# Optimization experiments

Measured on AMD Instinct MI355X. Metric: run time of the kernel, lower is better.

The kernel has to match this reference:

```python
import jax, jax.numpy as jnp
import numpy as np

IN_DIMS = 1024
K = 8


def setup_inputs() -> dict:
    key = jax.random.key(0)
    ks = jax.random.split(key, 7)
    s = 1.0 / np.sqrt(IN_DIMS)
    x = jax.random.normal(ks[0], (8, 2048, IN_DIMS), dtype=jnp.float32)
    Wq = jax.random.uniform(ks[1], (IN_DIMS, K), jnp.float32, -s, s)
    bq = jax.random.uniform(ks[2], (K,), jnp.float32, -s, s)
    Wk = jax.random.uniform(ks[3], (IN_DIMS, K), jnp.float32, -s, s)
    bk = jax.random.uniform(ks[4], (K,), jnp.float32, -s, s)
    Wv = jax.random.uniform(ks[5], (IN_DIMS, IN_DIMS), jnp.float32, -s, s)
    bv = jax.random.uniform(ks[6], (IN_DIMS,), jnp.float32, -s, s)
    return {"x": x, "Wq": Wq, "bq": bq, "Wk": Wk, "bk": bk, "Wv": Wv, "bv": bv}


def reference(x, Wq, bq, Wk, bk, Wv, bv):
    # x: [B,S,D]; rank-k projections
    q = jnp.einsum('bsd,dk->bsk', x, Wq) + bq        # [B,S,k]
    k = jnp.einsum('bsd,dk->bsk', x, Wk) + bk        # [B,S,k]
    energy = jnp.einsum('bik,bjk->bij', q, k)        # [B,S,S] (unscaled)
    attention = jax.nn.softmax(energy, axis=-1)
    value = jnp.einsum('bsd,de->bse', x, Wv) + bv    # [B,S,D]
    out = jnp.einsum('bij,bjd->bid', attention, value)
    return (out, attention)
```

## Files before the change

kernel.cpp:

```cpp
#include <hip/hip_runtime.h>


typedef __attribute__((ext_vector_type(8))) __bf16 bf16x8;
typedef __attribute__((ext_vector_type(4))) __bf16 bf16x4;
typedef __attribute__((ext_vector_type(4))) float  f32x4;
typedef unsigned int u32;

#define GLB_CAST(p) ((const __attribute__((address_space(1))) u32*)(p))
#define LDS_CAST(p) ((__attribute__((address_space(3))) u32*)(p))

#define S_BARRIER() { __builtin_amdgcn_s_barrier(); __builtin_amdgcn_sched_barrier(0); }
#define VMCNT8()    { asm volatile("s_waitcnt vmcnt(8)" ::: "memory"); __builtin_amdgcn_sched_barrier(0); }
#define VMCNT0()    { asm volatile("s_waitcnt vmcnt(0)" ::: "memory"); __builtin_amdgcn_sched_barrier(0); }

static constexpr int    Bn   = 8;
static constexpr int    S    = 2048;
static constexpr int    Dd   = 1024;
static constexpr int    Mtot = Bn * S;
static constexpr size_t OUT0 = (size_t)Bn * S * Dd;

static constexpr size_t OFF_XBF  = 0;
static constexpr size_t OFF_WVT  = OFF_XBF  + (size_t)Mtot * Dd * 2;
static constexpr size_t OFF_WQKT = OFF_WVT  + (size_t)Dd * Dd * 2;
static constexpr size_t OFF_Q    = OFF_WQKT + (size_t)16 * Dd * 2;
static constexpr size_t OFF_K    = OFF_Q    + (size_t)Mtot * 8 * 4;
static constexpr size_t OFF_VT   = OFF_K    + (size_t)Mtot * 8 * 4;
static constexpr size_t OFF_ATTB = OFF_VT   + (size_t)Bn * Dd * S * 2;
static constexpr size_t WS_NEED  = OFF_ATTB + (size_t)Bn * S * S * 2;

__global__ __launch_bounds__(256) void prep_kernel(
    const float* __restrict__ x, const float* __restrict__ Wq,
    const float* __restrict__ Wk, const float* __restrict__ Wv,
    __bf16* __restrict__ xbf, __bf16* __restrict__ wvt, __bf16* __restrict__ wqkT)
{
    __shared__ float lt[64][65];
    int bid = blockIdx.x, t = threadIdx.x;
    if (bid < 4096) {
        #pragma unroll
        for (int i = 0; i < 4; ++i) {
            size_t idx4 = (size_t)i * 1048576 + (size_t)bid * 256 + t;
            f32x4 v = ((const f32x4*)x)[idx4];
            bf16x4 o;
            #pragma unroll
            for (int c = 0; c < 4; ++c) o[c] = (__bf16)v[c];
            ((bf16x4*)xbf)[idx4] = o;
        }
    } else if (bid < 4352) {
        int tile = bid - 4096;
        int tr = tile >> 4, tc = tile & 15;
        int r0 = t >> 6, c = t & 63;
        #pragma unroll
        for (int i = 0; i < 16; ++i) {
            int row = i * 4 + r0;
            lt[row][c] = Wv[(size_t)(tr * 64 + row) * 1024 + tc * 64 + c];
        }
        __syncthreads();
        #pragma unroll
        for (int i = 0; i < 16; ++i) {
            int er = i * 4 + r0;
            wvt[(size_t)(tc * 64 + er) * 1024 + tr * 64 + c] = (__bf16)lt[c][er];
        }
    } else {
        int lb = bid - 4352;
        #pragma unroll
        for (int i = 0; i < 4; ++i) {
            int idx = (lb * 4 + i) * 256 + t;
            int n = idx >> 10, d = idx & 1023;
            float v = (n < 8) ? Wq[d * 8 + n] : Wk[d * 8 + (n & 7)];
            wqkT[n * 1024 + d] = (__bf16)v;
        }
    }
}

__global__ __launch_bounds__(256) void qk_proj_kernel(
    const __bf16* __restrict__ xbf, const __bf16* __restrict__ wqkT,
    const float* __restrict__ bq, const float* __restrict__ bk,
    float* __restrict__ qb, float* __restrict__ kb)
{
    int t = threadIdx.x, l = t & 63, w = t >> 6;
    int mbase = (blockIdx.x * 4 + w) * 16;
    f32x4 acc = {0.f, 0.f, 0.f, 0.f};
    const __bf16* ar = xbf + (size_t)(mbase + (l & 15)) * 1024 + ((l >> 4) << 3);
    const __bf16* br = wqkT + (size_t)(l & 15) * 1024 + ((l >> 4) << 3);
    #pragma unroll 8
    for (int kk = 0; kk < 1024; kk += 32) {
        bf16x8 a = *(const bf16x8*)(ar + kk);
        bf16x8 b = *(const bf16x8*)(br + kk);
        acc = __builtin_amdgcn_mfma_f32_16x16x32_bf16(a, b, acc, 0, 0, 0);
    }
    int n = l & 15;
    float bias = (n < 8) ? bq[n] : bk[n & 7];
    #pragma unroll
    for (int r = 0; r < 4; ++r) {
        int m = mbase + ((l >> 4) << 2) + r;
        float v = acc[r] + bias;
        if (n < 8) qb[m * 8 + n] = v;
        else       kb[m * 8 + (n & 7)] = v;
    }
}

__global__ __launch_bounds__(256) void softmax_kernel(
    const float* __restrict__ qb, const float* __restrict__ kb,
    float* __restrict__ attnF, __bf16* __restrict__ attnB)
{
    int bid = blockIdx.x;
    int b = bid >> 6, chunk = bid & 63;
    int t = threadIdx.x, l = t & 63, w = t >> 6;
    float kr[8][8];
    const float* kbb = kb + ((size_t)b << 14);
    #pragma unroll
    for (int jj = 0; jj < 8; ++jj) {
        f32x4 v0 = *(const f32x4*)(kbb + (size_t)(t * 8 + jj) * 8);
        f32x4 v1 = *(const f32x4*)(kbb + (size_t)(t * 8 + jj) * 8 + 4);
        #pragma unroll
        for (int c = 0; c < 4; ++c) { kr[jj][c] = v0[c]; kr[jj][4 + c] = v1[c]; }
    }
    __shared__ float redm[4], reds[4];
    const float* qrow = qb + ((size_t)b << 14);
    for (int ii = 0; ii < 32; ++ii) {
        int i = (chunk << 5) + ii;
        f32x4 q0 = *(const f32x4*)(qrow + (size_t)i * 8);
        f32x4 q1 = *(const f32x4*)(qrow + (size_t)i * 8 + 4);
        float e[8];
        #pragma unroll
        for (int jj = 0; jj < 8; ++jj) {
            float s = q0[0] * kr[jj][0];
            s = fmaf(q0[1], kr[jj][1], s);
            s = fmaf(q0[2], kr[jj][2], s);
            s = fmaf(q0[3], kr[jj][3], s);
            s = fmaf(q1[0], kr[jj][4], s);
            s = fmaf(q1[1], kr[jj][5], s);
            s = fmaf(q1[2], kr[jj][6], s);
            s = fmaf(q1[3], kr[jj][7], s);
            e[jj] = s;
        }
        float mx = e[0];
        #pragma unroll
        for (int jj = 1; jj < 8; ++jj) mx = fmaxf(mx, e[jj]);
        #pragma unroll
        for (int d = 1; d < 64; d <<= 1) mx = fmaxf(mx, __shfl_xor(mx, d));
        if (l == 0) redm[w] = mx;
        __syncthreads();
        mx = fmaxf(fmaxf(redm[0], redm[1]), fmaxf(redm[2], redm[3]));
        float p[8], sum = 0.f;
        #pragma unroll
        for (int jj = 0; jj < 8; ++jj) { p[jj] = __expf(e[jj] - mx); sum += p[jj]; }
        #pragma unroll
        for (int d = 1; d < 64; d <<= 1) sum += __shfl_xor(sum, d);
        if (l == 0) reds[w] = sum;
        __syncthreads();
        float T = (reds[0] + reds[1]) + (reds[2] + reds[3]);
        float inv = 1.0f / T;
        size_t off = (((size_t)b << 11) + i) * 2048 + (size_t)t * 8;
        f32x4 o0, o1; bf16x8 ob;
        #pragma unroll
        for (int c = 0; c < 4; ++c) {
            o0[c] = p[c] * inv; o1[c] = p[4 + c] * inv;
            ob[c] = (__bf16)o0[c]; ob[4 + c] = (__bf16)o1[c];
        }
        *(f32x4*)(attnF + off) = o0;
        *(f32x4*)(attnF + off + 4) = o1;
        *(bf16x8*)(attnB + off) = ob;
    }
}

template<int LDA>
__device__ __forceinline__ void stage_tile(const __bf16* Ab, const __bf16* Bb,
    char* smem, int slot, int kk, int rowin, int sl8, int wid)
{
    #pragma unroll
    for (int r = 0; r < 4; ++r) {
        __builtin_amdgcn_global_load_lds(
            GLB_CAST(Ab + (size_t)(r * 64 + rowin) * LDA + kk + sl8 * 8),
            LDS_CAST(smem + slot * 65536 + r * 8192 + wid * 1024), 16, 0, 0);
        __builtin_amdgcn_global_load_lds(
            GLB_CAST(Bb + (size_t)(r * 64 + rowin) * LDA + kk + sl8 * 8),
            LDS_CAST(smem + slot * 65536 + 32768 + r * 8192 + wid * 1024), 16, 0, 0);
    }
}

template<int MODE>
__global__ __launch_bounds__(512, 2) void gemm_kernel(
    const __bf16* __restrict__ A, const __bf16* __restrict__ Bt,
    float* __restrict__ outF, __bf16* __restrict__ outVt,
    const float* __restrict__ bv)
{
    constexpr int LDA = (MODE == 0) ? 1024 : 2048;
    constexpr int NT  = LDA / 64;
    __shared__ __align__(1024) char smem[131072];

    int bid = blockIdx.x;
    int wg = ((bid & 7) << 5) | (bid >> 3);
    int t = threadIdx.x, l = t & 63;
    int wid = t >> 6;
    int wmr = wid >> 2, wnc = wid & 3;

    int mblk, nblk, bb = 0;
    size_t aoff, boff;
    if constexpr (MODE == 0) {
        mblk = wg >> 2; nblk = wg & 3;
        aoff = (size_t)mblk * 256 * LDA; boff = 0;
    } else {
        bb = wg >> 5; int r = wg & 31;
        mblk = r >> 2; nblk = r & 3;
        aoff = (size_t)bb * S * S + (size_t)mblk * 256 * LDA;
        boff = (size_t)bb * Dd * S;
    }
    const __bf16* Ab = A + aoff;
    const __bf16* Bb = Bt + boff + (size_t)nblk * 256 * LDA;

    int rowin = t >> 3;
    int sl8 = (t & 7) ^ (rowin & 7);
    int lr = l & 15, lk = l >> 4;

    f32x4 acc[8][4] = {};

    stage_tile<LDA>(Ab, Bb, smem, 0, 0, rowin, sl8, wid);
    stage_tile<LDA>(Ab, Bb, smem, 1, 64, rowin, sl8, wid);
    VMCNT8();
    S_BARRIER();

    for (int tt = 0; tt < NT; ++tt) {
        int s = tt & 1;
        const __bf16* Asl = (const __bf16*)(smem + s * 65536);
        const __bf16* Bsl = (const __bf16*)(smem + s * 65536 + 32768);
        #pragma unroll
        for (int ks = 0; ks < 2; ++ks) {
            int sa = ks * 4 + lk;
            bf16x8 af[8], bfr[4];
            #pragma unroll
            for (int i = 0; i < 8; ++i) {
                int ra = wmr * 128 + i * 16 + lr;
                af[i] = *(const bf16x8*)&Asl[ra * 64 + ((sa ^ (ra & 7)) << 3)];
            }
            #pragma unroll
            for (int j = 0; j < 4; ++j) {
                int rb = wnc * 64 + j * 16 + lr;
                bfr[j] = *(const bf16x8*)&Bsl[rb * 64 + ((sa ^ (rb & 7)) << 3)];
            }
            __builtin_amdgcn_s_setprio(1);
            #pragma unroll
            for (int i = 0; i < 8; ++i)
                #pragma unroll
                for (int j = 0; j < 4; ++j)
                    acc[i][j] = __builtin_amdgcn_mfma_f32_16x16x32_bf16(af[i], bfr[j], acc[i][j], 0, 0, 0);
            __builtin_amdgcn_s_setprio(0);
        }
        if (tt == NT - 1) break;
        S_BARRIER();
        if (tt + 2 < NT) {
            stage_tile<LDA>(Ab, Bb, smem, s, (tt + 2) * 64, rowin, sl8, wid);
            VMCNT8();
        } else {
            VMCNT0();
        }
        S_BARRIER();
    }

    if constexpr (MODE == 0) {
        #pragma unroll
        for (int j = 0; j < 4; ++j) {
            int e = (nblk << 8) + wnc * 64 + j * 16 + lr;
            float bias = bv[e];
            #pragma unroll
            for (int i = 0; i < 8; ++i) {
                int m0 = (mblk << 8) + wmr * 128 + i * 16 + (lk << 2);
                int b = m0 >> 11, s0 = m0 & 2047;
                bf16x4 o;
                #pragma unroll
                for (int r = 0; r < 4; ++r) o[r] = (__bf16)(acc[i][j][r] + bias);
                *(bf16x4*)&outVt[(((size_t)(b << 10) + e) << 11) + s0] = o;
            }
        }
    } else {
        float* ob = outF + (size_t)bb * S * Dd;
        #pragma unroll
        for (int i = 0; i < 8; ++i) {
            int m0 = (mblk << 8) + wmr * 128 + i * 16 + (lk << 2);
            #pragma unroll
            for (int j = 0; j < 4; ++j) {
                int e = (nblk << 8) + wnc * 64 + j * 16 + lr;
                #pragma unroll
                for (int r = 0; r < 4; ++r)
                    ob[(size_t)(m0 + r) * 1024 + e] = acc[i][j][r];
            }
        }
    }
}

extern "C" void kernel_launch(void* const* d_in, const int* in_sizes, int n_in,
                              void* d_out, int out_size, void* d_ws, size_t ws_size,
                              hipStream_t stream)
{
    const float* x  = (const float*)d_in[0];
    const float* Wq = (const float*)d_in[1];
    const float* bq = (const float*)d_in[2];
    const float* Wk = (const float*)d_in[3];
    const float* bk = (const float*)d_in[4];
    const float* Wv = (const float*)d_in[5];
    const float* bv = (const float*)d_in[6];

    float* outp  = (float*)d_out;
    float* attnF = outp + OUT0;

    if (ws_size < WS_NEED) return;
    char* ws = (char*)d_ws;
    __bf16* xbf   = (__bf16*)(ws + OFF_XBF);
    __bf16* wvt   = (__bf16*)(ws + OFF_WVT);
    __bf16* wqkT  = (__bf16*)(ws + OFF_WQKT);
    float*  qbuf  = (float*)(ws + OFF_Q);
    float*  kbuf  = (float*)(ws + OFF_K);
    __bf16* vt    = (__bf16*)(ws + OFF_VT);
    __bf16* attnB = (__bf16*)(ws + OFF_ATTB);

    prep_kernel<<<4368, 256, 0, stream>>>(x, Wq, Wk, Wv, xbf, wvt, wqkT);
    qk_proj_kernel<<<256, 256, 0, stream>>>(xbf, wqkT, bq, bk, qbuf, kbuf);
    gemm_kernel<0><<<256, 512, 0, stream>>>(xbf, wvt, nullptr, vt, bv);
    softmax_kernel<<<512, 256, 0, stream>>>(qbuf, kbuf, attnF, attnB);
    gemm_kernel<1><<<256, 512, 0, stream>>>(attnB, vt, outp, nullptr, nullptr);
}
```

Before: 198.0 us.

## Split GEMM main loop into four quadrant phases interleaving prefetch with MFMA

The GEMM inner loop now splits the 8x4 MFMA tile into four quadrants. Each quadrant's LDS fragment reads are issued before the previous quadrant's MFMAs. The next tile's global-to-LDS loads are scattered across the phases once each slot's data has been consumed, instead of issued as a block after all compute. The aim is to overlap LDS reads and global prefetch with matrix math, at the cost of many more barriers per iteration and a finer-grained schedule that relies on correct slot reuse ordering.

Result: no change. 196.3 us (-0.9%).

```diff
diff --git a/kernel.cpp b/kernel.cpp
--- a/kernel.cpp
+++ b/kernel.cpp
@@ -10,6 +10,7 @@
 #define LDS_CAST(p) ((__attribute__((address_space(3))) u32*)(p))
 
 #define S_BARRIER() { __builtin_amdgcn_s_barrier(); __builtin_amdgcn_sched_barrier(0); }
+#define LGKM0()     { asm volatile("s_waitcnt lgkmcnt(0)" ::: "memory"); __builtin_amdgcn_sched_barrier(0); }
 #define VMCNT8()    { asm volatile("s_waitcnt vmcnt(8)" ::: "memory"); __builtin_amdgcn_sched_barrier(0); }
 #define VMCNT0()    { asm volatile("s_waitcnt vmcnt(0)" ::: "memory"); __builtin_amdgcn_sched_barrier(0); }
 
@@ -165,18 +166,20 @@
 }
 
 template<int LDA>
-__device__ __forceinline__ void stage_tile(const __bf16* Ab, const __bf16* Bb,
-    char* smem, int slot, int kk, int rowin, int sl8, int wid)
-{
-    #pragma unroll
-    for (int r = 0; r < 4; ++r) {
-        __builtin_amdgcn_global_load_lds(
-            GLB_CAST(Ab + (size_t)(r * 64 + rowin) * LDA + kk + sl8 * 8),
-            LDS_CAST(smem + slot * 65536 + r * 8192 + wid * 1024), 16, 0, 0);
-        __builtin_amdgcn_global_load_lds(
-            GLB_CAST(Bb + (size_t)(r * 64 + rowin) * LDA + kk + sl8 * 8),
-            LDS_CAST(smem + slot * 65536 + 32768 + r * 8192 + wid * 1024), 16, 0, 0);
-    }
+__device__ __forceinline__ void stageA(const __bf16* Ab, char* smem,
+    int slot, int kk, int c, int rowin, int sl8, int wid)
+{
+    __builtin_amdgcn_global_load_lds(
+        GLB_CAST(Ab + (size_t)(c * 64 + rowin) * LDA + kk + sl8 * 8),
+        LDS_CAST(smem + slot * 65536 + c * 8192 + wid * 1024), 16, 0, 0);
+}
+template<int LDA>
+__device__ __forceinline__ void stageB(const __bf16* Bb, char* smem,
+    int slot, int kk, int c, int rowin, int sl8, int wid)
+{
+    __builtin_amdgcn_global_load_lds(
+        GLB_CAST(Bb + (size_t)(c * 64 + rowin) * LDA + kk + sl8 * 8),
+        LDS_CAST(smem + slot * 65536 + 32768 + c * 8192 + wid * 1024), 16, 0, 0);
 }
 
 template<int MODE>
@@ -215,8 +218,16 @@
 
     f32x4 acc[8][4] = {};
 
-    stage_tile<LDA>(Ab, Bb, smem, 0, 0, rowin, sl8, wid);
-    stage_tile<LDA>(Ab, Bb, smem, 1, 64, rowin, sl8, wid);
+    #pragma unroll
+    for (int c = 0; c < 4; ++c) {
+        stageA<LDA>(Ab, smem, 0, 0, c, rowin, sl8, wid);
+        stageB<LDA>(Bb, smem, 0, 0, c, rowin, sl8, wid);
+    }
+    #pragma unroll
+    for (int c = 0; c < 4; ++c) {
+        stageA<LDA>(Ab, smem, 1, 64, c, rowin, sl8, wid);
+        stageB<LDA>(Bb, smem, 1, 64, c, rowin, sl8, wid);
+    }
     VMCNT8();
     S_BARRIER();
 
@@ -224,36 +235,106 @@
         int s = tt & 1;
         const __bf16* Asl = (const __bf16*)(smem + s * 65536);
         const __bf16* Bsl = (const __bf16*)(smem + s * 65536 + 32768);
+        bool pf = (tt + 2 < NT);
+        int kk2 = (tt + 2) * 64;
+
+        bf16x8 aLo[2][4], aHi[2][4], bLo[2][2], bHi[2][2];
+
         #pragma unroll
         for (int ks = 0; ks < 2; ++ks) {
             int sa = ks * 4 + lk;
-            bf16x8 af[8], bfr[4];
-            #pragma unroll
-            for (int i = 0; i < 8; ++i) {
+            #pragma unroll
+            for (int i = 0; i < 4; ++i) {
                 int ra = wmr * 128 + i * 16 + lr;
-                af[i] = *(const bf16x8*)&Asl[ra * 64 + ((sa ^ (ra & 7)) << 3)];
-            }
-            #pragma unroll
-            for (int j = 0; j < 4; ++j) {
+                aLo[ks][i] = *(const bf16x8*)&Asl[ra * 64 + ((sa ^ (ra & 7)) << 3)];
+            }
+            #pragma unroll
+            for (int j = 0; j < 2; ++j) {
                 int rb = wnc * 64 + j * 16 + lr;
-                bfr[j] = *(const bf16x8*)&Bsl[rb * 64 + ((sa ^ (rb & 7)) << 3)];
-            }
-            __builtin_amdgcn_s_setprio(1);
-            #pragma unroll
-            for (int i = 0; i < 8; ++i)
-                #pragma unroll
-                for (int j = 0; j < 4; ++j)
-                    acc[i][j] = __builtin_amdgcn_mfma_f32_16x16x32_bf16(af[i], bfr[j], acc[i][j], 0, 0, 0);
-            __builtin_amdgcn_s_setprio(0);
-        }
+                bLo[ks][j] = *(const bf16x8*)&Bsl[rb * 64 + ((sa ^ (rb & 7)) << 3)];
+            }
+        }
+        S_BARRIER(); LGKM0();
+        __builtin_amdgcn_s_setprio(1);
+        #pragma unroll
+        for (int ks = 0; ks < 2; ++ks)
+            #pragma unroll
+            for (int i = 0; i < 4; ++i)
+                #pragma unroll
+                for (int j = 0; j < 2; ++j)
+                    acc[i][j] = __builtin_amdgcn_mfma_f32_16x16x32_bf16(aLo[ks][i], bLo[ks][j], acc[i][j], 0, 0, 0);
+        __builtin_amdgcn_s_setprio(0);
+        S_BARRIER();
+
+        #pragma unroll
+        for (int ks = 0; ks < 2; ++ks) {
+            int sa = ks * 4 + lk;
+            #pragma unroll
+            for (int j = 0; j < 2; ++j) {
+                int rb = wnc * 64 + (j + 2) * 16 + lr;
+                bHi[ks][j] = *(const bf16x8*)&Bsl[rb * 64 + ((sa ^ (rb & 7)) << 3)];
+            }
+        }
+        if (pf) {
+            stageA<LDA>(Ab, smem, s, kk2, 0, rowin, sl8, wid);
+            stageA<LDA>(Ab, smem, s, kk2, 2, rowin, sl8, wid);
+        }
+        S_BARRIER(); LGKM0();
+        __builtin_amdgcn_s_setprio(1);
+        #pragma unroll
+        for (int ks = 0; ks < 2; ++ks)
+            #pragma unroll
+            for (int i = 0; i < 4; ++i)
+                #pragma unroll
+                for (int j = 0; j < 2; ++j)
+                    acc[i][2 + j] = __builtin_amdgcn_mfma_f32_16x16x32_bf16(aLo[ks][i], bHi[ks][j], acc[i][2 + j], 0, 0, 0);
+        __builtin_amdgcn_s_setprio(0);
+        S_BARRIER();
+
+        #pragma unroll
+        for (int ks = 0; ks < 2; ++ks) {
+            int sa = ks * 4 + lk;
+            #pragma unroll
+            for (int i = 0; i < 4; ++i) {
+                int ra = wmr * 128 + (i + 4) * 16 + lr;
+                aHi[ks][i] = *(const bf16x8*)&Asl[ra * 64 + ((sa ^ (ra & 7)) << 3)];
+            }
+        }
+        if (pf) {
+            #pragma unroll
+            for (int c = 0; c < 4; ++c)
+                stageB<LDA>(Bb, smem, s, kk2, c, rowin, sl8, wid);
+        }
+        S_BARRIER(); LGKM0();
+        __builtin_amdgcn_s_setprio(1);
+        #pragma unroll
+        for (int ks = 0; ks < 2; ++ks)
+            #pragma unroll
+            for (int i = 0; i < 4; ++i)
+                #pragma unroll
+                for (int j = 0; j < 2; ++j)
+                    acc[4 + i][2 + j] = __builtin_amdgcn_mfma_f32_16x16x32_bf16(aHi[ks][i], bHi[ks][j], acc[4 + i][2 + j], 0, 0, 0);
+        __builtin_amdgcn_s_setprio(0);
+        S_BARRIER();
+
+        if (pf) {
+            stageA<LDA>(Ab, smem, s, kk2, 1, rowin, sl8, wid);
+            stageA<LDA>(Ab, smem, s, kk2, 3, rowin, sl8, wid);
+        }
+        S_BARRIER();
+        __builtin_amdgcn_s_setprio(1);
+        #pragma unroll
+        for (int ks = 0; ks < 2; ++ks)
+            #pragma unroll
+            for (int i = 0; i < 4; ++i)
+                #pragma unroll
+                for (int j = 0; j < 2; ++j)
+                    acc[4 + i][j] = __builtin_amdgcn_mfma_f32_16x16x32_bf16(aHi[ks][i], bLo[ks][j], acc[4 + i][j], 0, 0, 0);
+        __builtin_amdgcn_s_setprio(0);
+
         if (tt == NT - 1) break;
         S_BARRIER();
-        if (tt + 2 < NT) {
-            stage_tile<LDA>(Ab, Bb, smem, s, (tt + 2) * 64, rowin, sl8, wid);
-            VMCNT8();
-        } else {
-            VMCNT0();
-        }
+        if (pf) { VMCNT8(); } else { VMCNT0(); }
         S_BARRIER();
     }
 
```

## Fuse QK projection into prep kernel and precompute GEMM LDS/global addresses

Applied to the files above, without the earlier changes.

Removes the separate qk_proj kernel and the wqkT transpose: the Q/K projection now runs inside prep_kernel, reading fp32 x directly and gathering Wq/Wk columns with strided loads converted to bf16 on the fly. This saves one kernel launch and a dependency on xbf. In the GEMM kernel, swizzled LDS offsets and global row pointers are hoisted out of the main loop to cut per-iteration address arithmetic. The cost is strided, uncoalesced weight loads in the projection blocks and some extra register pressure from the hoisted pointers.

New measurement: 200.1 us. No clear change (+1.1%).

```diff
diff --git a/kernel.cpp b/kernel.cpp
--- a/kernel.cpp
+++ b/kernel.cpp
@@ -20,33 +20,51 @@
 static constexpr size_t OUT0 = (size_t)Bn * S * Dd;
 
 static constexpr size_t OFF_XBF  = 0;
-static constexpr size_t OFF_WVT  = OFF_XBF  + (size_t)Mtot * Dd * 2;
-static constexpr size_t OFF_WQKT = OFF_WVT  + (size_t)Dd * Dd * 2;
-static constexpr size_t OFF_Q    = OFF_WQKT + (size_t)16 * Dd * 2;
-static constexpr size_t OFF_K    = OFF_Q    + (size_t)Mtot * 8 * 4;
-static constexpr size_t OFF_VT   = OFF_K    + (size_t)Mtot * 8 * 4;
-static constexpr size_t OFF_ATTB = OFF_VT   + (size_t)Bn * Dd * S * 2;
+static constexpr size_t OFF_WVT  = OFF_XBF + (size_t)Mtot * Dd * 2;
+static constexpr size_t OFF_Q    = OFF_WVT + (size_t)Dd * Dd * 2;
+static constexpr size_t OFF_K    = OFF_Q   + (size_t)Mtot * 8 * 4;
+static constexpr size_t OFF_VT   = OFF_K   + (size_t)Mtot * 8 * 4;
+static constexpr size_t OFF_ATTB = OFF_VT  + (size_t)Bn * Dd * S * 2;
 static constexpr size_t WS_NEED  = OFF_ATTB + (size_t)Bn * S * S * 2;
 
 __global__ __launch_bounds__(256) void prep_kernel(
     const float* __restrict__ x, const float* __restrict__ Wq,
     const float* __restrict__ Wk, const float* __restrict__ Wv,
-    __bf16* __restrict__ xbf, __bf16* __restrict__ wvt, __bf16* __restrict__ wqkT)
+    const float* __restrict__ bq, const float* __restrict__ bk,
+    __bf16* __restrict__ xbf, __bf16* __restrict__ wvt,
+    float* __restrict__ qb, float* __restrict__ kb)
 {
     __shared__ float lt[64][65];
     int bid = blockIdx.x, t = threadIdx.x;
-    if (bid < 4096) {
-        #pragma unroll
-        for (int i = 0; i < 4; ++i) {
-            size_t idx4 = (size_t)i * 1048576 + (size_t)bid * 256 + t;
-            f32x4 v = ((const f32x4*)x)[idx4];
-            bf16x4 o;
-            #pragma unroll
-            for (int c = 0; c < 4; ++c) o[c] = (__bf16)v[c];
-            ((bf16x4*)xbf)[idx4] = o;
-        }
-    } else if (bid < 4352) {
-        int tile = bid - 4096;
+    if (bid < 256) {
+        int l = t & 63, w = t >> 6;
+        int mbase = (bid * 4 + w) * 16;
+        int n = l & 15;
+        int dbase = (l >> 4) << 3;
+        const float* xr = x + (size_t)(mbase + n) * 1024 + dbase;
+        const float* wcol = (n < 8) ? (Wq + n) : (Wk + (n & 7));
+        f32x4 acc = {0.f, 0.f, 0.f, 0.f};
+        #pragma unroll 4
+        for (int kk = 0; kk < 1024; kk += 32) {
+            f32x4 a0 = *(const f32x4*)(xr + kk);
+            f32x4 a1 = *(const f32x4*)(xr + kk + 4);
+            bf16x8 a, b;
+            #pragma unroll
+            for (int c = 0; c < 4; ++c) { a[c] = (__bf16)a0[c]; a[4 + c] = (__bf16)a1[c]; }
+            #pragma unroll
+            for (int u = 0; u < 8; ++u) b[u] = (__bf16)wcol[(size_t)(dbase + kk + u) * 8];
+            acc = __builtin_amdgcn_mfma_f32_16x16x32_bf16(a, b, acc, 0, 0, 0);
+        }
+        float bias = (n < 8) ? bq[n] : bk[n & 7];
+        #pragma unroll
+        for (int r = 0; r < 4; ++r) {
+            int m = mbase + ((l >> 4) << 2) + r;
+            float v = acc[r] + bias;
+            if (n < 8) qb[m * 8 + n] = v;
+            else       kb[m * 8 + (n & 7)] = v;
+        }
+    } else if (bid < 512) {
+        int tile = bid - 256;
         int tr = tile >> 4, tc = tile & 15;
         int r0 = t >> 6, c = t & 63;
         #pragma unroll
@@ -61,41 +79,16 @@
             wvt[(size_t)(tc * 64 + er) * 1024 + tr * 64 + c] = (__bf16)lt[c][er];
         }
     } else {
-        int lb = bid - 4352;
+        int bid2 = bid - 512;
         #pragma unroll
         for (int i = 0; i < 4; ++i) {
-            int idx = (lb * 4 + i) * 256 + t;
-            int n = idx >> 10, d = idx & 1023;
-            float v = (n < 8) ? Wq[d * 8 + n] : Wk[d * 8 + (n & 7)];
-            wqkT[n * 1024 + d] = (__bf16)v;
-        }
-    }
-}
-
-__global__ __launch_bounds__(256) void qk_proj_kernel(
-    const __bf16* __restrict__ xbf, const __bf16* __restrict__ wqkT,
-    const float* __restrict__ bq, const float* __restrict__ bk,
-    float* __restrict__ qb, float* __restrict__ kb)
-{
-    int t = threadIdx.x, l = t & 63, w = t >> 6;
-    int mbase = (blockIdx.x * 4 + w) * 16;
-    f32x4 acc = {0.f, 0.f, 0.f, 0.f};
-    const __bf16* ar = xbf + (size_t)(mbase + (l & 15)) * 1024 + ((l >> 4) << 3);
-    const __bf16* br = wqkT + (size_t)(l & 15) * 1024 + ((l >> 4) << 3);
-    #pragma unroll 8
-    for (int kk = 0; kk < 1024; kk += 32) {
-        bf16x8 a = *(const bf16x8*)(ar + kk);
-        bf16x8 b = *(const bf16x8*)(br + kk);
-        acc = __builtin_amdgcn_mfma_f32_16x16x32_bf16(a, b, acc, 0, 0, 0);
-    }
-    int n = l & 15;
-    float bias = (n < 8) ? bq[n] : bk[n & 7];
-    #pragma unroll
-    for (int r = 0; r < 4; ++r) {
-        int m = mbase + ((l >> 4) << 2) + r;
-        float v = acc[r] + bias;
-        if (n < 8) qb[m * 8 + n] = v;
-        else       kb[m * 8 + (n & 7)] = v;
+            size_t idx4 = (size_t)i * 1048576 + (size_t)bid2 * 256 + t;
+            f32x4 v = ((const f32x4*)x)[idx4];
+            bf16x4 o;
+            #pragma unroll
+            for (int c = 0; c < 4; ++c) o[c] = (__bf16)v[c];
+            ((bf16x4*)xbf)[idx4] = o;
+        }
     }
 }
 
@@ -164,21 +157,6 @@
     }
 }
 
-template<int LDA>
-__device__ __forceinline__ void stage_tile(const __bf16* Ab, const __bf16* Bb,
-    char* smem, int slot, int kk, int rowin, int sl8, int wid)
-{
-    #pragma unroll
-    for (int r = 0; r < 4; ++r) {
-        __builtin_amdgcn_global_load_lds(
-            GLB_CAST(Ab + (size_t)(r * 64 + rowin) * LDA + kk + sl8 * 8),
-            LDS_CAST(smem + slot * 65536 + r * 8192 + wid * 1024), 16, 0, 0);
-        __builtin_amdgcn_global_load_lds(
-            GLB_CAST(Bb + (size_t)(r * 64 + rowin) * LDA + kk + sl8 * 8),
-            LDS_CAST(smem + slot * 65536 + 32768 + r * 8192 + wid * 1024), 16, 0, 0);
-    }
-}
-
 template<int MODE>
 __global__ __launch_bounds__(512, 2) void gemm_kernel(
     const __bf16* __restrict__ A, const __bf16* __restrict__ Bt,
@@ -213,43 +191,80 @@
     int sl8 = (t & 7) ^ (rowin & 7);
     int lr = l & 15, lk = l >> 4;
 
+    int slot0 = (lk ^ (lr & 7)) << 3;
+    int slot1 = ((lk ^ 4) ^ (lr & 7)) << 3;
+    int offA0 = (wmr * 128 + lr) * 64 + slot0;
+    int offA1 = (wmr * 128 + lr) * 64 + slot1;
+    int offB0 = (wnc * 64 + lr) * 64 + slot0;
+    int offB1 = (wnc * 64 + lr) * 64 + slot1;
+
+    const __bf16* gA[4]; const __bf16* gB[4];
+    #pragma unroll
+    for (int c = 0; c < 4; ++c) {
+        gA[c] = Ab + (size_t)(c * 64 + rowin) * LDA + sl8 * 8;
+        gB[c] = Bb + (size_t)(c * 64 + rowin) * LDA + sl8 * 8;
+    }
+
     f32x4 acc[8][4] = {};
 
-    stage_tile<LDA>(Ab, Bb, smem, 0, 0, rowin, sl8, wid);
-    stage_tile<LDA>(Ab, Bb, smem, 1, 64, rowin, sl8, wid);
+    #pragma unroll
+    for (int c = 0; c < 4; ++c) {
+        __builtin_amdgcn_global_load_lds(GLB_CAST(gA[c]),
+            LDS_CAST(smem + c * 8192 + wid * 1024), 16, 0, 0);
+        __builtin_amdgcn_global_load_lds(GLB_CAST(gB[c]),
+            LDS_CAST(smem + 32768 + c * 8192 + wid * 1024), 16, 0, 0);
+    }
+    #pragma unroll
+    for (int c = 0; c < 4; ++c) {
+        __builtin_amdgcn_global_load_lds(GLB_CAST(gA[c] + 64),
+            LDS_CAST(smem + 65536 + c * 8192 + wid * 1024), 16, 0, 0);
+        __builtin_amdgcn_global_load_lds(GLB_CAST(gB[c] + 64),
+            LDS_CAST(smem + 65536 + 32768 + c * 8192 + wid * 1024), 16, 0, 0);
+    }
     VMCNT8();
     S_BARRIER();
 
     for (int tt = 0; tt < NT; ++tt) {
-        int s = tt & 1;
-        const __bf16* Asl = (const __bf16*)(smem + s * 65536);
-        const __bf16* Bsl = (const __bf16*)(smem + s * 65536 + 32768);
-        #pragma unroll
-        for (int ks = 0; ks < 2; ++ks) {
-            int sa = ks * 4 + lk;
-            bf16x8 af[8], bfr[4];
-            #pragma unroll
-            for (int i = 0; i < 8; ++i) {
-                int ra = wmr * 128 + i * 16 + lr;
-                af[i] = *(const bf16x8*)&Asl[ra * 64 + ((sa ^ (ra & 7)) << 3)];
-            }
-            #pragma unroll
-            for (int j = 0; j < 4; ++j) {
-                int rb = wnc * 64 + j * 16 + lr;
-                bfr[j] = *(const bf16x8*)&Bsl[rb * 64 + ((sa ^ (rb & 7)) << 3)];
-            }
-            __builtin_amdgcn_s_setprio(1);
-            #pragma unroll
-            for (int i = 0; i < 8; ++i)
-                #pragma unroll
-                for (int j = 0; j < 4; ++j)
-                    acc[i][j] = __builtin_amdgcn_mfma_f32_16x16x32_bf16(af[i], bfr[j], acc[i][j], 0, 0, 0);
-            __builtin_amdgcn_s_setprio(0);
-        }
+        const __bf16* Asl = (const __bf16*)(smem + ((tt & 1) << 16));
+        const __bf16* Bsl = Asl + 16384;
+        bf16x8 af[8], bfr[4];
+
+        #pragma unroll
+        for (int i = 0; i < 8; ++i) af[i] = *(const bf16x8*)(Asl + offA0 + i * 1024);
+        #pragma unroll
+        for (int j = 0; j < 4; ++j) bfr[j] = *(const bf16x8*)(Bsl + offB0 + j * 1024);
+        __builtin_amdgcn_s_setprio(1);
+        #pragma unroll
+        for (int i = 0; i < 8; ++i)
+            #pragma unroll
+            for (int j = 0; j < 4; ++j)
+                acc[i][j] = __builtin_amdgcn_mfma_f32_16x16x32_bf16(af[i], bfr[j], acc[i][j], 0, 0, 0);
+        __builtin_amdgcn_s_setprio(0);
+
+        #pragma unroll
+        for (int i = 0; i < 8; ++i) af[i] = *(const bf16x8*)(Asl + offA1 + i * 1024);
+        #pragma unroll
+        for (int j = 0; j < 4; ++j) bfr[j] = *(const bf16x8*)(Bsl + offB1 + j * 1024);
+        __builtin_amdgcn_s_setprio(1);
+        #pragma unroll
+        for (int i = 0; i < 8; ++i)
+            #pragma unroll
+            for (int j = 0; j < 4; ++j)
+                acc[i][j] = __builtin_amdgcn_mfma_f32_16x16x32_bf16(af[i], bfr[j], acc[i][j], 0, 0, 0);
+        __builtin_amdgcn_s_setprio(0);
+
         if (tt == NT - 1) break;
         S_BARRIER();
         if (tt + 2 < NT) {
-            stage_tile<LDA>(Ab, Bb, smem, s, (tt + 2) * 64, rowin, sl8, wid);
+            int kk2 = (tt + 2) * 64;
+            char* dst = smem + ((tt & 1) << 16);
+            #pragma unroll
+            for (int c = 0; c < 4; ++c) {
+                __builtin_amdgcn_global_load_lds(GLB_CAST(gA[c] + kk2),
+                    LDS_CAST(dst + c * 8192 + wid * 1024), 16, 0, 0);
+                __builtin_amdgcn_global_load_lds(GLB_CAST(gB[c] + kk2),
+                    LDS_CAST(dst + 32768 + c * 8192 + wid * 1024), 16, 0, 0);
+            }
             VMCNT8();
         } else {
             VMCNT0();
@@ -257,14 +272,15 @@
         S_BARRIER();
     }
 
+    int lr2 = l & 15, lk2 = l >> 4;
     if constexpr (MODE == 0) {
         #pragma unroll
         for (int j = 0; j < 4; ++j) {
-            int e = (nblk << 8) + wnc * 64 + j * 16 + lr;
+            int e = (nblk << 8) + wnc * 64 + j * 16 + lr2;
             float bias = bv[e];
             #pragma unroll
             for (int i = 0; i < 8; ++i) {
-                int m0 = (mblk << 8) + wmr * 128 + i * 16 + (lk << 2);
+                int m0 = (mblk << 8) + wmr * 128 + i * 16 + (lk2 << 2);
                 int b = m0 >> 11, s0 = m0 & 2047;
                 bf16x4 o;
                 #pragma unroll
@@ -276,10 +292,10 @@
         float* ob = outF + (size_t)bb * S * Dd;
         #pragma unroll
         for (int i = 0; i < 8; ++i) {
-            int m0 = (mblk << 8) + wmr * 128 + i * 16 + (lk << 2);
+            int m0 = (mblk << 8) + wmr * 128 + i * 16 + (lk2 << 2);
             #pragma unroll
             for (int j = 0; j < 4; ++j) {
-                int e = (nblk << 8) + wnc * 64 + j * 16 + lr;
+                int e = (nblk << 8) + wnc * 64 + j * 16 + lr2;
                 #pragma unroll
                 for (int r = 0; r < 4; ++r)
                     ob[(size_t)(m0 + r) * 1024 + e] = acc[i][j][r];
@@ -307,14 +323,12 @@
     char* ws = (char*)d_ws;
     __bf16* xbf   = (__bf16*)(ws + OFF_XBF);
     __bf16* wvt   = (__bf16*)(ws + OFF_WVT);
-    __bf16* wqkT  = (__bf16*)(ws + OFF_WQKT);
     float*  qbuf  = (float*)(ws + OFF_Q);
     float*  kbuf  = (float*)(ws + OFF_K);
     __bf16* vt    = (__bf16*)(ws + OFF_VT);
     __bf16* attnB = (__bf16*)(ws + OFF_ATTB);
 
-    prep_kernel<<<4368, 256, 0, stream>>>(x, Wq, Wk, Wv, xbf, wvt, wqkT);
-    qk_proj_kernel<<<256, 256, 0, stream>>>(xbf, wqkT, bq, bk, qbuf, kbuf);
+    prep_kernel<<<4608, 256, 0, stream>>>(x, Wq, Wk, Wv, bq, bk, xbf, wvt, qbuf, kbuf);
     gemm_kernel<0><<<256, 512, 0, stream>>>(xbf, wvt, nullptr, vt, bv);
     softmax_kernel<<<512, 256, 0, stream>>>(qbuf, kbuf, attnF, attnB);
     gemm_kernel<1><<<256, 512, 0, stream>>>(attnB, vt, outp, nullptr, nullptr);
```
